# Kernel tuning notes

Hardware: AMD Instinct MI355X
Metric: run time of the kernel (lower is better)

The kernel has to match this reference:

```python
import jax, jax.numpy as jnp
import numpy as np

# SelectiveAttention (keras) reference.
# - A single shared InputDense (D -> key_dim) projects query, key, value.
# - ComponentBuilder yields (filter_input=Q, context_input=banded K^T, _input=V):
#   scores = (Q K^T / sqrt(key_dim)) masked to the band |i-j| <= band_size
#   (the layer's Softmax sublayer is built but never invoked in call()).
# - attended = scores @ V, then OutputDense (key_dim -> D). Dropout inactive at inference.

def setup_inputs() -> dict:
    key = jax.random.key(0)
    ks = jax.random.split(key, 5)
    B, S, D, Dk = 4, 4096, 512, 64
    query = jax.random.normal(ks[0], (B, S, D), dtype=jnp.float32)
    value = jax.random.normal(ks[1], (B, S, D), dtype=jnp.float32)
    Wi = jax.random.normal(ks[2], (D, Dk), dtype=jnp.float32) * (1.0 / np.sqrt(D))
    bi = jnp.zeros((Dk,), dtype=jnp.float32)
    Wo = jax.random.normal(ks[3], (Dk, D), dtype=jnp.float32) * (1.0 / np.sqrt(Dk))
    bo = jnp.zeros((D,), dtype=jnp.float32)
    return {"query": query, "value": value, "Wi": Wi, "bi": bi,
            "Wo": Wo, "bo": bo, "band_size": 128}


def reference(query, value, Wi, bi, Wo, bo, band_size):
    Dk = Wi.shape[1]
    scale = 1.0 / jnp.sqrt(jnp.asarray(Dk, dtype=query.dtype))
    # shared input projection (same dense for q, k, v; key defaults to value)
    q = query @ Wi + bi            # [B,S,Dk]
    kv = value @ Wi + bi           # [B,S,Dk]  (k == v here)
    scores = jnp.einsum('bqd,bkd->bqk', q, kv) * scale  # [B,S,S]
    S = q.shape[1]
    idx = jnp.arange(S)
    band = (jnp.abs(idx[:, None] - idx[None, :]) <= band_size)  # [S,S] bool
    scores = jnp.where(band[None], scores, 0.0)
    attended = jnp.einsum('bqk,bkd->bqd', scores, kv)    # [B,S,Dk]
    return attended @ Wo + bo                            # [B,S,D]
```

## Files before the change

kernel.cpp:

```cpp
#include <hip/hip_runtime.h>
#include <math.h>


typedef __bf16 bf16;
using bf16x8  = __attribute__((ext_vector_type(8))) __bf16;
using floatx4 = __attribute__((ext_vector_type(4))) float;

#define MFMA(a, b, c) __builtin_amdgcn_mfma_f32_16x16x32_bf16(a, b, c, 0, 0, 0)

__global__ __launch_bounds__(256) void prep_weights(
    const float* __restrict__ Wi, const float* __restrict__ Wo,
    bf16* __restrict__ WiT, bf16* __restrict__ WoT)
{
    __shared__ float T[64][65];
    const int blk = blockIdx.x, tid = threadIdx.x;
    if (blk < 8) {
        const int k0 = blk * 64;
        #pragma unroll
        for (int i = 0; i < 4; i++) {
            int idx4 = tid * 4 + i;
            int r = idx4 >> 4, c4 = (idx4 & 15) * 4;
            float4 f = *(const float4*)(Wi + (size_t)(k0 + r) * 64 + c4);
            T[r][c4 + 0] = f.x; T[r][c4 + 1] = f.y;
            T[r][c4 + 2] = f.z; T[r][c4 + 3] = f.w;
        }
        __syncthreads();
        #pragma unroll
        for (int i = 0; i < 2; i++) {
            int seg = tid * 2 + i;
            int n = seg >> 3, k8 = (seg & 7) * 8;
            bf16x8 v;
            #pragma unroll
            for (int j = 0; j < 8; j++) v[j] = (bf16)T[k8 + j][n];
            *(bf16x8*)(WiT + (size_t)n * 512 + k0 + k8) = v;
        }
    } else {
        const int n0 = (blk - 8) * 64;
        #pragma unroll
        for (int i = 0; i < 4; i++) {
            int idx4 = tid * 4 + i;
            int r = idx4 >> 4, c4 = (idx4 & 15) * 4;
            float4 f = *(const float4*)(Wo + (size_t)r * 512 + n0 + c4);
            T[r][c4 + 0] = f.x; T[r][c4 + 1] = f.y;
            T[r][c4 + 2] = f.z; T[r][c4 + 3] = f.w;
        }
        __syncthreads();
        #pragma unroll
        for (int i = 0; i < 2; i++) {
            int seg = tid * 2 + i;
            int n = seg >> 3, k8 = (seg & 7) * 8;
            bf16x8 v;
            #pragma unroll
            for (int j = 0; j < 8; j++) v[j] = (bf16)T[k8 + j][n];
            *(bf16x8*)(WoT + (size_t)(n0 + n) * 64 + k8) = v;
        }
    }
}

__global__ __launch_bounds__(256, 2) void proj_in_kernel(
    const float* __restrict__ q, const float* __restrict__ v,
    const bf16* __restrict__ WiT, const float* __restrict__ bi,
    bf16* __restrict__ qp, bf16* __restrict__ kvp, int K)
{
    const float* x = blockIdx.z ? v : q;
    bf16* y = blockIdx.z ? kvp : qp;
    const int tid = threadIdx.x;
    const int wave = tid >> 6, lane = tid & 63;
    const int lr = lane & 15, lq = lane >> 4;
    const int row0 = (blockIdx.x * 4 + wave) * 16;
    const float* xrow = x + (size_t)(row0 + lr) * K;

    floatx4 acc[4] = {};
    #pragma unroll
    for (int ks = 0; ks < 16; ks++) {
        const int k0 = ks * 32 + lq * 8;
        float4 a0 = *(const float4*)(xrow + k0);
        float4 a1 = *(const float4*)(xrow + k0 + 4);
        bf16x8 af;
        af[0] = (bf16)a0.x; af[1] = (bf16)a0.y; af[2] = (bf16)a0.z; af[3] = (bf16)a0.w;
        af[4] = (bf16)a1.x; af[5] = (bf16)a1.y; af[6] = (bf16)a1.z; af[7] = (bf16)a1.w;
        #pragma unroll
        for (int t = 0; t < 4; t++) {
            bf16x8 bf = *(const bf16x8*)(WiT + (size_t)(t * 16 + lr) * K + k0);
            acc[t] = MFMA(af, bf, acc[t]);
        }
    }
    #pragma unroll
    for (int t = 0; t < 4; t++) {
        float b = bi[t * 16 + lr];
        #pragma unroll
        for (int r = 0; r < 4; r++)
            y[(size_t)(row0 + lq * 4 + r) * 64 + t * 16 + lr] = (bf16)(acc[t][r] + b);
    }
}

__global__ __launch_bounds__(256) void transpose_kv(
    const bf16* __restrict__ kvp, bf16* __restrict__ kvT, int S)
{
    const int b = blockIdx.y, s0 = blockIdx.x * 64;
    __shared__ bf16 L[64][66];
    const int tid = threadIdx.x;
    #pragma unroll
    for (int i = 0; i < 2; i++) {
        int seg = tid * 2 + i;
        int s = seg >> 3, d0 = (seg & 7) * 8;
        bf16x8 vv = *(const bf16x8*)(kvp + ((size_t)b * S + s0 + s) * 64 + d0);
        #pragma unroll
        for (int j = 0; j < 8; j++) L[d0 + j][s] = vv[j];
    }
    __syncthreads();
    #pragma unroll
    for (int i = 0; i < 2; i++) {
        int seg = tid * 2 + i;
        int d = seg >> 3, so = (seg & 7) * 8;
        bf16x8 vv;
        #pragma unroll
        for (int j = 0; j < 8; j++) vv[j] = L[d][so + j];
        *(bf16x8*)(kvT + ((size_t)b * 64 + d) * S + s0 + so) = vv;
    }
}

__global__ __launch_bounds__(256) void band_attn_kernel(
    const bf16* __restrict__ qp, const bf16* __restrict__ kvp,
    const bf16* __restrict__ kvT, const int* __restrict__ band_ptr,
    float* __restrict__ att, int S, float scale)
{
    __shared__ bf16 Ss[4][2][16][88];
    const int tid = threadIdx.x;
    const int wave = tid >> 6, lane = tid & 63;
    const int lr = lane & 15, lq = lane >> 4;
    const int gw = blockIdx.x * 4 + wave;
    const int b = gw >> 8;
    const int q0 = (gw & 255) * 16;
    const int band = band_ptr[0];

    const bf16* qb = qp + ((size_t)b * S + q0) * 64;
    bf16x8 qf0 = *(const bf16x8*)(qb + lr * 64 + lq * 8);
    bf16x8 qf1 = *(const bf16x8*)(qb + lr * 64 + 32 + lq * 8);

    floatx4 acc[4] = {};
    const int ch_lo = (q0 - band) >> 6;
    #pragma unroll
    for (int cc = 0; cc < 5; cc++) {
        const int kj0 = (ch_lo + cc) * 64;
        bf16 (*strip)[88] = Ss[wave][cc & 1];
        floatx4 sc[4] = {};
        #pragma unroll
        for (int t = 0; t < 4; t++) {
            int kr = kj0 + t * 16 + lr;
            int krc = min(max(kr, 0), S - 1);
            const bf16* kp = kvp + ((size_t)b * S + krc) * 64;
            bf16x8 b0 = *(const bf16x8*)(kp + lq * 8);
            bf16x8 b1 = *(const bf16x8*)(kp + 32 + lq * 8);
            sc[t] = MFMA(qf0, b0, sc[t]);
            sc[t] = MFMA(qf1, b1, sc[t]);
        }
        #pragma unroll
        for (int t = 0; t < 4; t++) {
            int kj = kj0 + t * 16 + lr;
            bool kv_ok = (kj >= 0) && (kj < S);
            #pragma unroll
            for (int r = 0; r < 4; r++) {
                int qi = q0 + lq * 4 + r;
                int dlt = qi - kj; dlt = dlt < 0 ? -dlt : dlt;
                float vv = (kv_ok && dlt <= band) ? sc[t][r] * scale : 0.f;
                strip[lq * 4 + r][t * 16 + lr] = (bf16)vv;
            }
        }
        #pragma unroll
        for (int ks = 0; ks < 2; ks++) {
            bf16x8 sa = *(const bf16x8*)(&strip[lr][ks * 32 + lq * 8]);
            int kb = kj0 + ks * 32 + lq * 8;
            int kbc = min(max(kb, 0), S - 8);
            #pragma unroll
            for (int t = 0; t < 4; t++) {
                bf16x8 vb = *(const bf16x8*)(kvT + ((size_t)b * 64 + t * 16 + lr) * S + kbc);
                acc[t] = MFMA(sa, vb, acc[t]);
            }
        }
    }
    #pragma unroll
    for (int t = 0; t < 4; t++)
        #pragma unroll
        for (int r = 0; r < 4; r++)
            att[((size_t)b * S + q0 + lq * 4 + r) * 64 + t * 16 + lr] = acc[t][r];
}

__global__ __launch_bounds__(256, 4) void proj_out_kernel(
    const float* __restrict__ att, const bf16* __restrict__ WoT,
    const float* __restrict__ bo, float* __restrict__ out, int D)
{
    const int tid = threadIdx.x;
    const int wave = tid >> 6, lane = tid & 63;
    const int lr = lane & 15, lq = lane >> 4;
    const int row0 = blockIdx.x * 64 + wave * 16;
    const int n0 = blockIdx.y * 128;
    const float* ar = att + (size_t)(row0 + lr) * 64;

    bf16x8 af[2];
    #pragma unroll
    for (int ks = 0; ks < 2; ks++) {
        float4 a0 = *(const float4*)(ar + ks * 32 + lq * 8);
        float4 a1 = *(const float4*)(ar + ks * 32 + lq * 8 + 4);
        af[ks][0] = (bf16)a0.x; af[ks][1] = (bf16)a0.y;
        af[ks][2] = (bf16)a0.z; af[ks][3] = (bf16)a0.w;
        af[ks][4] = (bf16)a1.x; af[ks][5] = (bf16)a1.y;
        af[ks][6] = (bf16)a1.z; af[ks][7] = (bf16)a1.w;
    }
    floatx4 acc[8] = {};
    #pragma unroll
    for (int t = 0; t < 8; t++) {
        #pragma unroll
        for (int ks = 0; ks < 2; ks++) {
            bf16x8 bf = *(const bf16x8*)(WoT + (size_t)(n0 + t * 16 + lr) * 64 + ks * 32 + lq * 8);
            acc[t] = MFMA(af[ks], bf, acc[t]);
        }
    }
    #pragma unroll
    for (int t = 0; t < 8; t++) {
        float b = bo[n0 + t * 16 + lr];
        #pragma unroll
        for (int r = 0; r < 4; r++)
            out[(size_t)(row0 + lq * 4 + r) * D + n0 + t * 16 + lr] = acc[t][r] + b;
    }
}

extern "C" void kernel_launch(void* const* d_in, const int* in_sizes, int n_in,
                              void* d_out, int out_size, void* d_ws, size_t ws_size,
                              hipStream_t stream) {
    const float* query = (const float*)d_in[0];
    const float* value = (const float*)d_in[1];
    const float* Wi    = (const float*)d_in[2];
    const float* bi    = (const float*)d_in[3];
    const float* Wo    = (const float*)d_in[4];
    const float* bo    = (const float*)d_in[5];
    const int*   band  = (const int*)d_in[6];
    float* out = (float*)d_out;

    const int Dk = in_sizes[3];
    const int D  = in_sizes[5];
    const int S  = 4096;
    const int BS = in_sizes[0] / D;
    const int B  = BS / S;
    const float scale = 1.0f / sqrtf((float)Dk);

    bf16* WiT = (bf16*)d_ws;
    bf16* WoT = WiT + 32768;
    bf16* qp  = WoT + 32768;
    bf16* kvp = qp  + (size_t)BS * 64;
    bf16* kvT = kvp + (size_t)BS * 64;
    float* attb = (float*)(kvT + (size_t)BS * 64);

    prep_weights<<<16, 256, 0, stream>>>(Wi, Wo, WiT, WoT);

    proj_in_kernel<<<dim3(BS / 64, 1, 2), 256, 0, stream>>>(
        query, value, WiT, bi, qp, kvp, D);

    transpose_kv<<<dim3(S / 64, B), 256, 0, stream>>>(kvp, kvT, S);

    band_attn_kernel<<<dim3(BS / 64), 256, 0, stream>>>(
        qp, kvp, kvT, band, attb, S, scale);

    proj_out_kernel<<<dim3(BS / 64, D / 128), 256, 0, stream>>>(
        attb, WoT, bo, out, D);
}
```

Before: 158.3 us.

## Fuse KV transpose into input projection and output projection into band attention

The input projection now splits the K dimension across the four waves of a block (16 rows per block), reduces the partial sums through shared memory, and writes both the row-major kvp and the transposed kvT directly, so the separate transpose kernel goes away. The output projection is fused into the band-attention kernel: each wave packs its attended tile to bf16 in shared memory and multiplies it by WoT in-kernel. This removes the fp32 att round trip and two kernel launches. In exchange there is an extra shared-memory reduction and sync in the projection, and the per-wave output loop has more serial work.

```diff
diff --git a/kernel.cpp b/kernel.cpp
--- a/kernel.cpp
+++ b/kernel.cpp
@@ -3,6 +3,7 @@
 
 
 typedef __bf16 bf16;
+using bf16x4  = __attribute__((ext_vector_type(4))) __bf16;
 using bf16x8  = __attribute__((ext_vector_type(8))) __bf16;
 using floatx4 = __attribute__((ext_vector_type(4))) float;
 
@@ -57,22 +58,25 @@
     }
 }
 
-__global__ __launch_bounds__(256, 2) void proj_in_kernel(
+__global__ __launch_bounds__(256) void proj_in_kernel(
     const float* __restrict__ q, const float* __restrict__ v,
     const bf16* __restrict__ WiT, const float* __restrict__ bi,
-    bf16* __restrict__ qp, bf16* __restrict__ kvp, int K)
+    bf16* __restrict__ qp, bf16* __restrict__ kvp, bf16* __restrict__ kvT,
+    int K, int S)
 {
     const float* x = blockIdx.z ? v : q;
     bf16* y = blockIdx.z ? kvp : qp;
+    __shared__ float P[4][16][68];
     const int tid = threadIdx.x;
     const int wave = tid >> 6, lane = tid & 63;
     const int lr = lane & 15, lq = lane >> 4;
-    const int row0 = (blockIdx.x * 4 + wave) * 16;
-    const float* xrow = x + (size_t)(row0 + lr) * K;
+    const int row0 = blockIdx.x * 16;
+    const float* xrow = x + (size_t)(row0 + lr) * K + wave * 128;
+    const bf16* wrow = WiT + wave * 128;
 
     floatx4 acc[4] = {};
     #pragma unroll
-    for (int ks = 0; ks < 16; ks++) {
+    for (int ks = 0; ks < 4; ks++) {
         const int k0 = ks * 32 + lq * 8;
         float4 a0 = *(const float4*)(xrow + k0);
         float4 a1 = *(const float4*)(xrow + k0 + 4);
@@ -81,49 +85,51 @@
         af[4] = (bf16)a1.x; af[5] = (bf16)a1.y; af[6] = (bf16)a1.z; af[7] = (bf16)a1.w;
         #pragma unroll
         for (int t = 0; t < 4; t++) {
-            bf16x8 bf = *(const bf16x8*)(WiT + (size_t)(t * 16 + lr) * K + k0);
-            acc[t] = MFMA(af, bf, acc[t]);
-        }
-    }
-    #pragma unroll
-    for (int t = 0; t < 4; t++) {
-        float b = bi[t * 16 + lr];
+            bf16x8 bfv = *(const bf16x8*)(wrow + (size_t)(t * 16 + lr) * K + k0);
+            acc[t] = MFMA(af, bfv, acc[t]);
+        }
+    }
+    #pragma unroll
+    for (int t = 0; t < 4; t++)
         #pragma unroll
         for (int r = 0; r < 4; r++)
-            y[(size_t)(row0 + lq * 4 + r) * 64 + t * 16 + lr] = (bf16)(acc[t][r] + b);
-    }
-}
-
-__global__ __launch_bounds__(256) void transpose_kv(
-    const bf16* __restrict__ kvp, bf16* __restrict__ kvT, int S)
-{
-    const int b = blockIdx.y, s0 = blockIdx.x * 64;
-    __shared__ bf16 L[64][66];
-    const int tid = threadIdx.x;
-    #pragma unroll
-    for (int i = 0; i < 2; i++) {
-        int seg = tid * 2 + i;
-        int s = seg >> 3, d0 = (seg & 7) * 8;
-        bf16x8 vv = *(const bf16x8*)(kvp + ((size_t)b * S + s0 + s) * 64 + d0);
-        #pragma unroll
-        for (int j = 0; j < 8; j++) L[d0 + j][s] = vv[j];
-    }
+            P[wave][lq * 4 + r][t * 16 + lr] = acc[t][r];
     __syncthreads();
-    #pragma unroll
-    for (int i = 0; i < 2; i++) {
-        int seg = tid * 2 + i;
-        int d = seg >> 3, so = (seg & 7) * 8;
-        bf16x8 vv;
-        #pragma unroll
-        for (int j = 0; j < 8; j++) vv[j] = L[d][so + j];
-        *(bf16x8*)(kvT + ((size_t)b * 64 + d) * S + s0 + so) = vv;
-    }
-}
-
-__global__ __launch_bounds__(256) void band_attn_kernel(
+
+    {
+        const int row = tid >> 4, c4 = (tid & 15) * 4;
+        float4 s0 = *(const float4*)&P[0][row][c4];
+        float4 s1 = *(const float4*)&P[1][row][c4];
+        float4 s2 = *(const float4*)&P[2][row][c4];
+        float4 s3 = *(const float4*)&P[3][row][c4];
+        float4 bb = *(const float4*)(bi + c4);
+        bf16x4 o;
+        o[0] = (bf16)(s0.x + s1.x + s2.x + s3.x + bb.x);
+        o[1] = (bf16)(s0.y + s1.y + s2.y + s3.y + bb.y);
+        o[2] = (bf16)(s0.z + s1.z + s2.z + s3.z + bb.z);
+        o[3] = (bf16)(s0.w + s1.w + s2.w + s3.w + bb.w);
+        *(bf16x4*)(y + (size_t)(row0 + row) * 64 + c4) = o;
+    }
+    if (blockIdx.z) {
+        const int d = tid >> 2, s4 = (tid & 3) * 4;
+        const int b = row0 >> 12, s0r = row0 & (S - 1);
+        const float bb = bi[d];
+        bf16x4 o;
+        #pragma unroll
+        for (int i = 0; i < 4; i++) {
+            float s = P[0][s4 + i][d] + P[1][s4 + i][d]
+                    + P[2][s4 + i][d] + P[3][s4 + i][d] + bb;
+            o[i] = (bf16)s;
+        }
+        *(bf16x4*)(kvT + ((size_t)b * 64 + d) * S + s0r + s4) = o;
+    }
+}
+
+__global__ __launch_bounds__(256) void band_attn_out_kernel(
     const bf16* __restrict__ qp, const bf16* __restrict__ kvp,
     const bf16* __restrict__ kvT, const int* __restrict__ band_ptr,
-    float* __restrict__ att, int S, float scale)
+    const bf16* __restrict__ WoT, const float* __restrict__ bo,
+    float* __restrict__ out, int S, float scale)
 {
     __shared__ bf16 Ss[4][2][16][88];
     const int tid = threadIdx.x;
@@ -179,49 +185,28 @@
             }
         }
     }
+
+    bf16 (*strip)[88] = Ss[wave][0];
     #pragma unroll
     for (int t = 0; t < 4; t++)
         #pragma unroll
         for (int r = 0; r < 4; r++)
-            att[((size_t)b * S + q0 + lq * 4 + r) * 64 + t * 16 + lr] = acc[t][r];
-}
-
-__global__ __launch_bounds__(256, 4) void proj_out_kernel(
-    const float* __restrict__ att, const bf16* __restrict__ WoT,
-    const float* __restrict__ bo, float* __restrict__ out, int D)
-{
-    const int tid = threadIdx.x;
-    const int wave = tid >> 6, lane = tid & 63;
-    const int lr = lane & 15, lq = lane >> 4;
-    const int row0 = blockIdx.x * 64 + wave * 16;
-    const int n0 = blockIdx.y * 128;
-    const float* ar = att + (size_t)(row0 + lr) * 64;
-
-    bf16x8 af[2];
-    #pragma unroll
-    for (int ks = 0; ks < 2; ks++) {
-        float4 a0 = *(const float4*)(ar + ks * 32 + lq * 8);
-        float4 a1 = *(const float4*)(ar + ks * 32 + lq * 8 + 4);
-        af[ks][0] = (bf16)a0.x; af[ks][1] = (bf16)a0.y;
-        af[ks][2] = (bf16)a0.z; af[ks][3] = (bf16)a0.w;
-        af[ks][4] = (bf16)a1.x; af[ks][5] = (bf16)a1.y;
-        af[ks][6] = (bf16)a1.z; af[ks][7] = (bf16)a1.w;
-    }
-    floatx4 acc[8] = {};
-    #pragma unroll
-    for (int t = 0; t < 8; t++) {
-        #pragma unroll
-        for (int ks = 0; ks < 2; ks++) {
-            bf16x8 bf = *(const bf16x8*)(WoT + (size_t)(n0 + t * 16 + lr) * 64 + ks * 32 + lq * 8);
-            acc[t] = MFMA(af[ks], bf, acc[t]);
-        }
-    }
-    #pragma unroll
-    for (int t = 0; t < 8; t++) {
-        float b = bo[n0 + t * 16 + lr];
+            strip[lq * 4 + r][t * 16 + lr] = (bf16)acc[t][r];
+    bf16x8 af0 = *(const bf16x8*)(&strip[lr][lq * 8]);
+    bf16x8 af1 = *(const bf16x8*)(&strip[lr][32 + lq * 8]);
+    float* orow = out + ((size_t)b * S + q0) * 512;
+    #pragma unroll 8
+    for (int tp = 0; tp < 32; tp++) {
+        const bf16* wp = WoT + (size_t)(tp * 16 + lr) * 64;
+        bf16x8 b0 = *(const bf16x8*)(wp + lq * 8);
+        bf16x8 b1 = *(const bf16x8*)(wp + 32 + lq * 8);
+        floatx4 o = {};
+        o = MFMA(af0, b0, o);
+        o = MFMA(af1, b1, o);
+        float bb = bo[tp * 16 + lr];
         #pragma unroll
         for (int r = 0; r < 4; r++)
-            out[(size_t)(row0 + lq * 4 + r) * D + n0 + t * 16 + lr] = acc[t][r] + b;
+            orow[(size_t)(lq * 4 + r) * 512 + tp * 16 + lr] = o[r] + bb;
     }
 }
 
@@ -249,18 +234,12 @@
     bf16* qp  = WoT + 32768;
     bf16* kvp = qp  + (size_t)BS * 64;
     bf16* kvT = kvp + (size_t)BS * 64;
-    float* attb = (float*)(kvT + (size_t)BS * 64);
 
     prep_weights<<<16, 256, 0, stream>>>(Wi, Wo, WiT, WoT);
 
-    proj_in_kernel<<<dim3(BS / 64, 1, 2), 256, 0, stream>>>(
-        query, value, WiT, bi, qp, kvp, D);
-
-    transpose_kv<<<dim3(S / 64, B), 256, 0, stream>>>(kvp, kvT, S);
-
-    band_attn_kernel<<<dim3(BS / 64), 256, 0, stream>>>(
-        qp, kvp, kvT, band, attb, S, scale);
-
-    proj_out_kernel<<<dim3(BS / 64, D / 128), 256, 0, stream>>>(
-        attb, WoT, bo, out, D);
-}
+    proj_in_kernel<<<dim3(BS / 16, 1, 2), 256, 0, stream>>>(
+        query, value, WiT, bi, qp, kvp, kvT, D, S);
+
+    band_attn_out_kernel<<<dim3(BS / 64), 256, 0, stream>>>(
+        qp, kvp, kvT, band, WoT, bo, out, S, scale);
+}
```

After: 150.9 us. -4.7%, faster.
